# Performance work log

Measured on AMD Instinct MI355X. Metric: run time of the kernel, lower is better.

The kernel has to match this reference:

```python
import jax, jax.numpy as jnp
import numpy as np

IN_FEATURES = 4096
OUT_FEATURES = 11008
LUT_SIZE = 256
N_TOKENS = 64


def setup_inputs() -> dict:
    key = jax.random.key(0)
    k1, k2, k3, k4 = jax.random.split(key, 4)
    x = jax.random.normal(k1, (N_TOKENS, IN_FEATURES), dtype=jnp.float32)
    grid_indices = jax.random.randint(k2, (OUT_FEATURES, IN_FEATURES), 0, LUT_SIZE, dtype=jnp.int32)
    lut = jax.random.normal(k3, (LUT_SIZE,), dtype=jnp.float32)
    scale = jax.random.uniform(k4, (OUT_FEATURES, 1), dtype=jnp.float32)
    return {"x": x, "grid_indices": grid_indices, "lut": lut, "scale": scale}


def reference(x, grid_indices, lut, scale):
    # Dequantize weight: LUT gather per element, then per-output-row scale.
    # weight: [out_features, in_features]
    weight = lut[grid_indices] * scale
    # F.linear(x, W) == x @ W.T ; out: [n_tokens, out_features]
    return jnp.einsum('ti,oi->to', x, weight)
```

## Files before the change

### kernel.cpp

```cpp
#include <hip/hip_runtime.h>
#include <stdint.h>

#define N_TOK 64
#define K_DIM 4096
#define N_OUT 11008
#define LUT_N 256

typedef __attribute__((ext_vector_type(4))) float  floatx4;
typedef __attribute__((ext_vector_type(8))) __bf16 bf16x8;

__device__ __forceinline__ unsigned bf16_rne(float f) {
  unsigned u = __builtin_bit_cast(unsigned, f);
  return (u + 0x7fffu + ((u >> 16) & 1u)) >> 16;
}

__global__ __launch_bounds__(256) void xcvt_kernel(const float* __restrict__ x,
                                                   unsigned short* __restrict__ xb) {
  int i = (blockIdx.x * 256 + threadIdx.x) * 4;
  float4 v = *(const float4*)(x + i);
  ushort4 o;
  o.x = (unsigned short)bf16_rne(v.x);
  o.y = (unsigned short)bf16_rne(v.y);
  o.z = (unsigned short)bf16_rne(v.z);
  o.w = (unsigned short)bf16_rne(v.w);
  *(ushort4*)(xb + i) = o;
}

template <bool XB>
__global__ __launch_bounds__(256, 3) void ghost_kernel(
    const float* __restrict__ x, const int* __restrict__ gidx,
    const float* __restrict__ lut, const float* __restrict__ scale,
    const unsigned short* __restrict__ xb, float* __restrict__ out) {
  __shared__ unsigned lut_lds[LUT_N * 16];
  __shared__ floatx4 red[4][4][64];

  const int tid = threadIdx.x;
  {
    unsigned hb = bf16_rne(lut[tid]);
#pragma unroll
    for (int c = 0; c < 16; ++c) lut_lds[tid * 16 + c] = hb;
  }
  __syncthreads();

  const int w    = tid >> 6;
  const int lane = tid & 63;
  const int m15  = lane & 15;
  const int q    = lane >> 4;
  const int o    = blockIdx.x * 16 + m15;
  const int kw0  = w * 1024;

  const int* idxp = gidx + (size_t)o * K_DIM + kw0 + q * 8;

  floatx4 acc[4];
#pragma unroll
  for (int tt = 0; tt < 4; ++tt) acc[tt] = (floatx4){0.f, 0.f, 0.f, 0.f};

  int4 buf[2][4];
#pragma unroll
  for (int s = 0; s < 2; ++s) {
    buf[0][2 * s + 0] = *(const int4*)(idxp + 32 * s);
    buf[0][2 * s + 1] = *(const int4*)(idxp + 32 * s + 4);
  }

#pragma unroll 2
  for (int win = 0; win < 16; ++win) {
    const int cu = win & 1, nx = cu ^ 1;
    if (win < 15) {
      const int* p = idxp + (win + 1) * 64;
#pragma unroll
      for (int s = 0; s < 2; ++s) {
        buf[nx][2 * s + 0] = *(const int4*)(p + 32 * s);
        buf[nx][2 * s + 1] = *(const int4*)(p + 32 * s + 4);
      }
    }

    uint4  axb[4][2];
    float4 axf[4][2][2];
#pragma unroll
    for (int tt = 0; tt < 4; ++tt)
#pragma unroll
      for (int s = 0; s < 2; ++s) {
        const int e = (tt * 16 + m15) * K_DIM + kw0 + win * 64 + 32 * s + 8 * q;
        if constexpr (XB) {
          axb[tt][s] = *(const uint4*)(xb + e);
        } else {
          axf[tt][s][0] = *(const float4*)(x + e);
          axf[tt][s][1] = *(const float4*)(x + e + 4);
        }
      }

#pragma unroll
    for (int s = 0; s < 2; ++s) {
      const int4 i0 = buf[cu][2 * s + 0];
      const int4 i1 = buf[cu][2 * s + 1];
      unsigned g0 = lut_lds[i0.x * 16 + m15];
      unsigned g1 = lut_lds[i0.y * 16 + m15];
      unsigned g2 = lut_lds[i0.z * 16 + m15];
      unsigned g3 = lut_lds[i0.w * 16 + m15];
      unsigned g4 = lut_lds[i1.x * 16 + m15];
      unsigned g5 = lut_lds[i1.y * 16 + m15];
      unsigned g6 = lut_lds[i1.z * 16 + m15];
      unsigned g7 = lut_lds[i1.w * 16 + m15];
      uint4 bi;
      bi.x = __builtin_amdgcn_perm(g1, g0, 0x05040100u);
      bi.y = __builtin_amdgcn_perm(g3, g2, 0x05040100u);
      bi.z = __builtin_amdgcn_perm(g5, g4, 0x05040100u);
      bi.w = __builtin_amdgcn_perm(g7, g6, 0x05040100u);
      bf16x8 bfrag = __builtin_bit_cast(bf16x8, bi);

#pragma unroll
      for (int tt = 0; tt < 4; ++tt) {
        bf16x8 afrag;
        if constexpr (XB) {
          afrag = __builtin_bit_cast(bf16x8, axb[tt][s]);
        } else {
          const float4 lo = axf[tt][s][0], hi = axf[tt][s][1];
          uint4 ai;
          ai.x = __builtin_amdgcn_perm(__builtin_bit_cast(unsigned, lo.y),
                                       __builtin_bit_cast(unsigned, lo.x), 0x07060302u);
          ai.y = __builtin_amdgcn_perm(__builtin_bit_cast(unsigned, lo.w),
                                       __builtin_bit_cast(unsigned, lo.z), 0x07060302u);
          ai.z = __builtin_amdgcn_perm(__builtin_bit_cast(unsigned, hi.y),
                                       __builtin_bit_cast(unsigned, hi.x), 0x07060302u);
          ai.w = __builtin_amdgcn_perm(__builtin_bit_cast(unsigned, hi.w),
                                       __builtin_bit_cast(unsigned, hi.z), 0x07060302u);
          afrag = __builtin_bit_cast(bf16x8, ai);
        }
        acc[tt] = __builtin_amdgcn_mfma_f32_16x16x32_bf16(afrag, bfrag, acc[tt], 0, 0, 0);
      }
    }
  }

  __syncthreads();
#pragma unroll
  for (int tt = 0; tt < 4; ++tt) red[w][tt][lane] = acc[tt];
  __syncthreads();
  {
    floatx4 r = red[0][w][lane];
    r += red[1][w][lane];
    r += red[2][w][lane];
    r += red[3][w][lane];
    const float sc = scale[blockIdx.x * 16 + m15];
    r *= sc;
#pragma unroll
    for (int i = 0; i < 4; ++i)
      out[(size_t)(16 * w + q * 4 + i) * N_OUT + blockIdx.x * 16 + m15] = r[i];
  }
}

extern "C" void kernel_launch(void* const* d_in, const int* in_sizes, int n_in,
                              void* d_out, int out_size, void* d_ws, size_t ws_size,
                              hipStream_t stream) {
  const float* x   = (const float*)d_in[0];
  const int*   gi  = (const int*)d_in[1];
  const float* lut = (const float*)d_in[2];
  const float* sc  = (const float*)d_in[3];
  float*       out = (float*)d_out;

  const size_t xb_bytes = (size_t)N_TOK * K_DIM * sizeof(unsigned short);
  if (ws_size >= xb_bytes) {
    unsigned short* xb = (unsigned short*)d_ws;
    xcvt_kernel<<<(N_TOK * K_DIM) / (256 * 4), 256, 0, stream>>>(x, xb);
    ghost_kernel<true><<<N_OUT / 16, 256, 0, stream>>>(x, gi, lut, sc, xb, out);
  } else {
    ghost_kernel<false><<<N_OUT / 16, 256, 0, stream>>>(x, gi, lut, sc, nullptr, out);
  }
}
```

Measured before the change: 279.7 us.

## Pre-pack activations into MFMA fragment order and deepen index prefetch pipeline

The conversion kernel now writes bf16 activations already permuted into the per-lane MFMA fragment layout, so the main kernel reads them as fully coalesced contiguous uint4 loads instead of strided row gathers. The main loop is restructured into 32 steps with a 4-deep register ring buffer prefetching both index and activation fragments. The fp32 fallback path is removed, so the workspace is now assumed to be large enough. Register pressure rises with the deeper buffers, which may affect the 3-blocks-per-CU occupancy target.

```diff
diff --git a/kernel.cpp b/kernel.cpp
--- a/kernel.cpp
+++ b/kernel.cpp
@@ -14,23 +14,27 @@
   return (u + 0x7fffu + ((u >> 16) & 1u)) >> 16;
 }
 
-__global__ __launch_bounds__(256) void xcvt_kernel(const float* __restrict__ x,
-                                                   unsigned short* __restrict__ xb) {
-  int i = (blockIdx.x * 256 + threadIdx.x) * 4;
-  float4 v = *(const float4*)(x + i);
-  ushort4 o;
-  o.x = (unsigned short)bf16_rne(v.x);
-  o.y = (unsigned short)bf16_rne(v.y);
-  o.z = (unsigned short)bf16_rne(v.z);
-  o.w = (unsigned short)bf16_rne(v.w);
-  *(ushort4*)(xb + i) = o;
+__global__ __launch_bounds__(256) void xpack_kernel(const float* __restrict__ x,
+                                                    uint32_t* __restrict__ xp) {
+  const int t = blockIdx.x * 256 + threadIdx.x;
+  const int lane = t & 63, c = t >> 6;
+  const int m15 = lane & 15, q = lane >> 4;
+  const int tt = c & 3, st = (c >> 2) & 31, w = c >> 7;
+  const int src = (tt * 16 + m15) * K_DIM + w * 1024 + st * 32 + q * 8;
+  float4 a = *(const float4*)(x + src);
+  float4 b = *(const float4*)(x + src + 4);
+  uint4 o;
+  o.x = bf16_rne(a.x) | (bf16_rne(a.y) << 16);
+  o.y = bf16_rne(a.z) | (bf16_rne(a.w) << 16);
+  o.z = bf16_rne(b.x) | (bf16_rne(b.y) << 16);
+  o.w = bf16_rne(b.z) | (bf16_rne(b.w) << 16);
+  *(uint4*)(xp + (size_t)t * 4) = o;
 }
 
-template <bool XB>
 __global__ __launch_bounds__(256, 3) void ghost_kernel(
-    const float* __restrict__ x, const int* __restrict__ gidx,
-    const float* __restrict__ lut, const float* __restrict__ scale,
-    const unsigned short* __restrict__ xb, float* __restrict__ out) {
+    const int* __restrict__ gidx, const float* __restrict__ lut,
+    const float* __restrict__ scale, const uint32_t* __restrict__ xp,
+    float* __restrict__ out) {
   __shared__ unsigned lut_lds[LUT_N * 16];
   __shared__ floatx4 red[4][4][64];
 
@@ -42,93 +46,62 @@
   }
   __syncthreads();
 
-  const int w    = tid >> 6;
-  const int lane = tid & 63;
-  const int m15  = lane & 15;
-  const int q    = lane >> 4;
-  const int o    = blockIdx.x * 16 + m15;
-  const int kw0  = w * 1024;
+  const int w = tid >> 6, lane = tid & 63;
+  const int m15 = lane & 15, q = lane >> 4;
+  const int o = blockIdx.x * 16 + m15;
 
-  const int* idxp = gidx + (size_t)o * K_DIM + kw0 + q * 8;
+  const int* idxp = gidx + (size_t)o * K_DIM + w * 1024 + q * 8;
+  const uint4* ap = (const uint4*)xp + (size_t)w * 32 * 4 * 64 + lane;
 
   floatx4 acc[4];
 #pragma unroll
   for (int tt = 0; tt < 4; ++tt) acc[tt] = (floatx4){0.f, 0.f, 0.f, 0.f};
 
-  int4 buf[2][4];
+  int4  ib[4][2];
+  uint4 ab[4][4];
 #pragma unroll
-  for (int s = 0; s < 2; ++s) {
-    buf[0][2 * s + 0] = *(const int4*)(idxp + 32 * s);
-    buf[0][2 * s + 1] = *(const int4*)(idxp + 32 * s + 4);
+  for (int p = 0; p < 4; ++p) {
+    ib[p][0] = *(const int4*)(idxp + p * 32);
+    ib[p][1] = *(const int4*)(idxp + p * 32 + 4);
+#pragma unroll
+    for (int tt = 0; tt < 4; ++tt) ab[p][tt] = ap[(p * 4 + tt) * 64];
   }
 
-#pragma unroll 2
-  for (int win = 0; win < 16; ++win) {
-    const int cu = win & 1, nx = cu ^ 1;
-    if (win < 15) {
-      const int* p = idxp + (win + 1) * 64;
+#pragma unroll 4
+  for (int st = 0; st < 32; ++st) {
+    const int p = st & 3;
+    const int4 i0 = ib[p][0], i1 = ib[p][1];
+    uint4 a0 = ab[p][0], a1 = ab[p][1], a2 = ab[p][2], a3 = ab[p][3];
+    if (st < 28) {
+      ib[p][0] = *(const int4*)(idxp + (st + 4) * 32);
+      ib[p][1] = *(const int4*)(idxp + (st + 4) * 32 + 4);
 #pragma unroll
-      for (int s = 0; s < 2; ++s) {
-        buf[nx][2 * s + 0] = *(const int4*)(p + 32 * s);
-        buf[nx][2 * s + 1] = *(const int4*)(p + 32 * s + 4);
-      }
+      for (int tt = 0; tt < 4; ++tt) ab[p][tt] = ap[((st + 4) * 4 + tt) * 64];
     }
 
-    uint4  axb[4][2];
-    float4 axf[4][2][2];
-#pragma unroll
-    for (int tt = 0; tt < 4; ++tt)
-#pragma unroll
-      for (int s = 0; s < 2; ++s) {
-        const int e = (tt * 16 + m15) * K_DIM + kw0 + win * 64 + 32 * s + 8 * q;
-        if constexpr (XB) {
-          axb[tt][s] = *(const uint4*)(xb + e);
-        } else {
-          axf[tt][s][0] = *(const float4*)(x + e);
-          axf[tt][s][1] = *(const float4*)(x + e + 4);
-        }
-      }
+    unsigned g0 = lut_lds[i0.x * 16 + m15];
+    unsigned g1 = lut_lds[i0.y * 16 + m15];
+    unsigned g2 = lut_lds[i0.z * 16 + m15];
+    unsigned g3 = lut_lds[i0.w * 16 + m15];
+    unsigned g4 = lut_lds[i1.x * 16 + m15];
+    unsigned g5 = lut_lds[i1.y * 16 + m15];
+    unsigned g6 = lut_lds[i1.z * 16 + m15];
+    unsigned g7 = lut_lds[i1.w * 16 + m15];
+    uint4 bi;
+    bi.x = __builtin_amdgcn_perm(g1, g0, 0x05040100u);
+    bi.y = __builtin_amdgcn_perm(g3, g2, 0x05040100u);
+    bi.z = __builtin_amdgcn_perm(g5, g4, 0x05040100u);
+    bi.w = __builtin_amdgcn_perm(g7, g6, 0x05040100u);
+    const bf16x8 bfrag = __builtin_bit_cast(bf16x8, bi);
 
-#pragma unroll
-    for (int s = 0; s < 2; ++s) {
-      const int4 i0 = buf[cu][2 * s + 0];
-      const int4 i1 = buf[cu][2 * s + 1];
-      unsigned g0 = lut_lds[i0.x * 16 + m15];
-      unsigned g1 = lut_lds[i0.y * 16 + m15];
-      unsigned g2 = lut_lds[i0.z * 16 + m15];
-      unsigned g3 = lut_lds[i0.w * 16 + m15];
-      unsigned g4 = lut_lds[i1.x * 16 + m15];
-      unsigned g5 = lut_lds[i1.y * 16 + m15];
-      unsigned g6 = lut_lds[i1.z * 16 + m15];
-      unsigned g7 = lut_lds[i1.w * 16 + m15];
-      uint4 bi;
-      bi.x = __builtin_amdgcn_perm(g1, g0, 0x05040100u);
-      bi.y = __builtin_amdgcn_perm(g3, g2, 0x05040100u);
-      bi.z = __builtin_amdgcn_perm(g5, g4, 0x05040100u);
-      bi.w = __builtin_amdgcn_perm(g7, g6, 0x05040100u);
-      bf16x8 bfrag = __builtin_bit_cast(bf16x8, bi);
-
-#pragma unroll
-      for (int tt = 0; tt < 4; ++tt) {
-        bf16x8 afrag;
-        if constexpr (XB) {
-          afrag = __builtin_bit_cast(bf16x8, axb[tt][s]);
-        } else {
-          const float4 lo = axf[tt][s][0], hi = axf[tt][s][1];
-          uint4 ai;
-          ai.x = __builtin_amdgcn_perm(__builtin_bit_cast(unsigned, lo.y),
-                                       __builtin_bit_cast(unsigned, lo.x), 0x07060302u);
-          ai.y = __builtin_amdgcn_perm(__builtin_bit_cast(unsigned, lo.w),
-                                       __builtin_bit_cast(unsigned, lo.z), 0x07060302u);
-          ai.z = __builtin_amdgcn_perm(__builtin_bit_cast(unsigned, hi.y),
-                                       __builtin_bit_cast(unsigned, hi.x), 0x07060302u);
-          ai.w = __builtin_amdgcn_perm(__builtin_bit_cast(unsigned, hi.w),
-                                       __builtin_bit_cast(unsigned, hi.z), 0x07060302u);
-          afrag = __builtin_bit_cast(bf16x8, ai);
-        }
-        acc[tt] = __builtin_amdgcn_mfma_f32_16x16x32_bf16(afrag, bfrag, acc[tt], 0, 0, 0);
-      }
-    }
+    acc[0] = __builtin_amdgcn_mfma_f32_16x16x32_bf16(
+        __builtin_bit_cast(bf16x8, a0), bfrag, acc[0], 0, 0, 0);
+    acc[1] = __builtin_amdgcn_mfma_f32_16x16x32_bf16(
+        __builtin_bit_cast(bf16x8, a1), bfrag, acc[1], 0, 0, 0);
+    acc[2] = __builtin_amdgcn_mfma_f32_16x16x32_bf16(
+        __builtin_bit_cast(bf16x8, a2), bfrag, acc[2], 0, 0, 0);
+    acc[3] = __builtin_amdgcn_mfma_f32_16x16x32_bf16(
+        __builtin_bit_cast(bf16x8, a3), bfrag, acc[3], 0, 0, 0);
   }
 
   __syncthreads();
@@ -157,12 +130,7 @@
   const float* sc  = (const float*)d_in[3];
   float*       out = (float*)d_out;
 
-  const size_t xb_bytes = (size_t)N_TOK * K_DIM * sizeof(unsigned short);
-  if (ws_size >= xb_bytes) {
-    unsigned short* xb = (unsigned short*)d_ws;
-    xcvt_kernel<<<(N_TOK * K_DIM) / (256 * 4), 256, 0, stream>>>(x, xb);
-    ghost_kernel<true><<<N_OUT / 16, 256, 0, stream>>>(x, gi, lut, sc, xb, out);
-  } else {
-    ghost_kernel<false><<<N_OUT / 16, 256, 0, stream>>>(x, gi, lut, sc, nullptr, out);
-  }
+  uint32_t* xp = (uint32_t*)d_ws;
+  xpack_kernel<<<(N_TOK * K_DIM / 8) / 256, 256, 0, stream>>>(x, xp);
+  ghost_kernel<<<N_OUT / 16, 256, 0, stream>>>(gi, lut, sc, xp, out);
 }
```

Result: faster. 273.6 us (-2.2%).
